# Kernel optimization log

Hardware: AMD Instinct MI355X
Metric: run time of the kernel (lower is better)

## Reference

```python
import jax, jax.numpy as jnp
import numpy as np

N = 50000
HID = 128
NH = 4
E_RES, E_SEQ, E_KNN = 100000, 100000, 200000
BN_EPS = 1e-5
NEG_SLOPE = 0.2


def _gat(h, src, dst, W, al, ar, resW, b):
    """DGL-style GATConv (eval mode: feat_drop off, residual=True, bias).
    h: (N, in), W/resW: (in, H*out), al/ar: (H, out), b: (H*out,)"""
    Hh, out = al.shape
    feat = (h @ W).reshape(N, Hh, out)                 # (N, H, out)
    el = jnp.sum(feat * al, axis=-1)                   # (N, H)
    er = jnp.sum(feat * ar, axis=-1)                   # (N, H)
    e = jax.nn.leaky_relu(el[src] + er[dst], NEG_SLOPE)  # (E, H)
    # edge softmax over incoming edges of each dst node (numerically stable)
    m = jax.ops.segment_max(e, dst, num_segments=N)    # (N, H)
    ex = jnp.exp(e - m[dst])
    s = jax.ops.segment_sum(ex, dst, num_segments=N)
    a = ex / s[dst]                                    # (E, H)
    msg = a[:, :, None] * feat[src]                    # (E, H, out)
    rst = jax.ops.segment_sum(msg, dst, num_segments=N)  # (N, H, out)
    return rst + (h @ resW).reshape(N, Hh, out) + b.reshape(1, Hh, out)


def _hetero(h, src_res, dst_res, src_seq, dst_seq, src_knn, dst_knn, W, al, ar, resW, b):
    # HeteroGraphConv with aggregate='sum' over relations, then mean over heads
    r = _gat(h, src_res, dst_res, W[0], al[0], ar[0], resW[0], b[0])
    r = r + _gat(h, src_seq, dst_seq, W[1], al[1], ar[1], resW[1], b[1])
    r = r + _gat(h, src_knn, dst_knn, W[2], al[2], ar[2], resW[2], b[2])
    return jnp.mean(r, axis=1)                         # (N, out)


def setup_inputs() -> dict:
    key = jax.random.key(0)
    ks = iter(jax.random.split(key, 32))
    inp = {}
    inp["x"] = jax.random.normal(next(ks), (N, HID), jnp.float32)
    inp["src_res"] = jax.random.randint(next(ks), (E_RES,), 0, N, jnp.int32)
    inp["dst_res"] = jax.random.randint(next(ks), (E_RES,), 0, N, jnp.int32)
    inp["src_seq"] = jax.random.randint(next(ks), (E_SEQ,), 0, N, jnp.int32)
    inp["dst_seq"] = jax.random.randint(next(ks), (E_SEQ,), 0, N, jnp.int32)
    inp["src_knn"] = jax.random.randint(next(ks), (E_KNN,), 0, N, jnp.int32)
    inp["dst_knn"] = jax.random.randint(next(ks), (E_KNN,), 0, N, jnp.int32)
    sc = 0.05
    for l in (0, 1):
        inp[f"W{l}"] = jax.random.normal(next(ks), (3, HID, NH * HID), jnp.float32) * sc
        inp[f"al{l}"] = jax.random.normal(next(ks), (3, NH, HID), jnp.float32) * sc
        inp[f"ar{l}"] = jax.random.normal(next(ks), (3, NH, HID), jnp.float32) * sc
        inp[f"resW{l}"] = jax.random.normal(next(ks), (3, HID, NH * HID), jnp.float32) * sc
        inp[f"b{l}"] = jax.random.normal(next(ks), (3, NH * HID), jnp.float32) * sc
    inp["fc_W"] = jax.random.normal(next(ks), (HID, HID), jnp.float32) * sc
    inp["fc_b"] = jax.random.normal(next(ks), (HID,), jnp.float32) * sc
    inp["bn_gamma"] = jnp.ones((HID,), jnp.float32)
    inp["bn_beta"] = jnp.zeros((HID,), jnp.float32)
    inp["bn_mean"] = jax.random.normal(next(ks), (HID,), jnp.float32) * sc
    inp["bn_var"] = jax.random.uniform(next(ks), (HID,), jnp.float32)
    return inp


def reference(x, src_res, dst_res, src_seq, dst_seq, src_knn, dst_knn,
              W0, al0, ar0, resW0, b0, W1, al1, ar1, resW1, b1,
              fc_W, fc_b, bn_gamma, bn_beta, bn_mean, bn_var):
    # layer 0: hetero GAT, head-mean, fc + ReLU + BatchNorm (eval), dropout=identity
    h = _hetero(x, src_res, dst_res, src_seq, dst_seq, src_knn, dst_knn,
                W0, al0, ar0, resW0, b0)
    h = jax.nn.relu(h @ fc_W + fc_b)
    h = (h - bn_mean) / jnp.sqrt(bn_var + BN_EPS) * bn_gamma + bn_beta
    # layer 1 (final): hetero GAT, head-mean
    out = _hetero(h, src_res, dst_res, src_seq, dst_seq, src_knn, dst_knn,
                  W1, al1, ar1, resW1, b1)
    return out
```

## Files before the change

kernel.cpp:

```cpp
#include <hip/hip_runtime.h>
#include <hip/hip_bf16.h>
#include <math.h>
#include <stdint.h>

#define NNODES 50000
#define SCHUNK 4096
#define AW 1664
#define XOFF 1536

typedef __bf16 bf16x8 __attribute__((ext_vector_type(8)));
typedef float f32x4 __attribute__((ext_vector_type(4)));
typedef unsigned short u16;
typedef unsigned int u32;

__device__ __forceinline__ float lrelu(float x){ return x >= 0.f ? x : 0.2f*x; }
__device__ __forceinline__ float lo2f(u32 v){ union{ u32 i; float f; } c; c.i = v<<16; return c.f; }
__device__ __forceinline__ float hi2f(u32 v){ union{ u32 i; float f; } c; c.i = v & 0xffff0000u; return c.f; }
__device__ __forceinline__ u16 f2b(float f){ __hip_bfloat16 h = __float2bfloat16(f); return *(u16*)&h; }
__device__ __forceinline__ u32 packbf(float a, float b){ return (u32)f2b(a) | ((u32)f2b(b) << 16); }

#define GLDS16(g, l) __builtin_amdgcn_global_load_lds( \
    (const __attribute__((address_space(1))) void*)(g), \
    (__attribute__((address_space(3))) void*)(l), 16, 0, 0)

__global__ void prep_all(const float* __restrict__ W0, const float* __restrict__ W1,
                         const float* __restrict__ resW0, const float* __restrict__ resW1,
                         const float* __restrict__ b0, const float* __restrict__ b1,
                         const float* __restrict__ al0, const float* __restrict__ ar0,
                         const float* __restrict__ al1, const float* __restrict__ ar1,
                         const float* __restrict__ fcW,
                         u16* __restrict__ Btb, float* __restrict__ biasf,
                         u16* __restrict__ wlb, u16* __restrict__ fcWtb,
                         int* __restrict__ cnt)
{
    int gid = blockIdx.x*blockDim.x + threadIdx.x;
    if (gid < 3*NNODES) cnt[gid] = 0;
    if (gid < 2*128*AW){
        int l = gid / (128*AW);
        int rem = gid - l*(128*AW);
        int c = rem / AW;
        int j = rem - c*AW;
        const float* W  = l ? W1 : W0;
        const float* rw = l ? resW1 : resW0;
        float v;
        if (j < XOFF){
            int r = j >> 9, h = (j >> 7) & 3, k = j & 127;
            v = 0.25f * W[(size_t)r*65536 + (size_t)k*512 + h*128 + c];
        } else {
            int k = j - XOFF;
            float s = 0.f;
            for (int r = 0; r < 3; ++r)
                for (int h = 0; h < 4; ++h)
                    s += rw[(size_t)r*65536 + (size_t)k*512 + h*128 + c];
            v = 0.25f * s;
        }
        Btb[gid] = f2b(v);
    }
    if (gid < 256){
        int l = gid >> 7, c = gid & 127;
        const float* bb = l ? b1 : b0;
        float s = 0.f;
        for (int r = 0; r < 3; ++r)
            for (int h = 0; h < 4; ++h)
                s += bb[r*512 + h*128 + c];
        biasf[gid] = 0.25f*s;
    }
    if (gid < 2*128*128){
        int l = gid >> 14;
        int col = (gid >> 7) & 127;
        int k = gid & 127;
        float v = 0.f;
        if (col < 24){
            int r = col >> 3, lr = (col >> 2) & 1, h = col & 3;
            const float* W = l ? W1 : W0;
            const float* av = l ? (lr ? ar1 : al1) : (lr ? ar0 : al0);
            const float* wrow = W + (size_t)r*65536 + (size_t)k*512 + h*128;
            const float* arow = av + r*512 + h*128;
            for (int cc = 0; cc < 128; ++cc) v += wrow[cc]*arow[cc];
        }
        wlb[gid] = f2b(v);
    }
    if (gid < 128*128){
        int k = gid & 127, n = gid >> 7;
        fcWtb[gid] = f2b(fcW[k*128 + n]);
    }
}

__global__ __launch_bounds__(256) void xprep_kernel(const float* __restrict__ x,
    u16* __restrict__ Ax, const u16* __restrict__ wl, float* __restrict__ el, int M)
{
    __shared__ u16 Xs[64*136];
    __shared__ u16 Ws[32*136];
    const int tid = threadIdx.x;
    const int row0 = blockIdx.x*64;
    #pragma unroll
    for (int p = 0; p < 2; ++p){
        int idx = tid + p*256;
        int c = idx >> 4, kc = (idx & 15)*8;
        float4 v = make_float4(0.f,0.f,0.f,0.f);
        if (c < 24) v = *(const float4*)(wl + c*128 + kc);
        *(float4*)&Ws[c*136 + kc] = v;
    }
    int r = tid >> 2, cq = (tid & 3)*32;
    int grow = row0 + r;
    if (grow < M){
        #pragma unroll
        for (int i = 0; i < 8; ++i){
            float4 v = *(const float4*)(x + (size_t)grow*128 + cq + i*4);
            ushort4 o;
            o.x = f2b(v.x); o.y = f2b(v.y); o.z = f2b(v.z); o.w = f2b(v.w);
            *(ushort4*)(Ax + (size_t)grow*AW + cq + i*4) = o;
            *(ushort4*)&Xs[r*136 + cq + i*4] = o;
        }
    } else {
        ushort4 z; z.x=0; z.y=0; z.z=0; z.w=0;
        #pragma unroll
        for (int i = 0; i < 8; ++i) *(ushort4*)&Xs[r*136 + cq + i*4] = z;
    }
    __syncthreads();
    const int lane = tid & 63, wave = tid >> 6;
    const int r16 = lane & 15, quad = lane >> 4;
    f32x4 acc0 = {}, acc1 = {};
    #pragma unroll
    for (int ks = 0; ks < 4; ++ks){
        int ko = ks*32 + quad*8;
        bf16x8 a  = *(const bf16x8*)&Xs[(wave*16 + r16)*136 + ko];
        bf16x8 b0 = *(const bf16x8*)&Ws[r16*136 + ko];
        bf16x8 b1 = *(const bf16x8*)&Ws[(16 + r16)*136 + ko];
        acc0 = __builtin_amdgcn_mfma_f32_16x16x32_bf16(a, b0, acc0, 0,0,0);
        acc1 = __builtin_amdgcn_mfma_f32_16x16x32_bf16(a, b1, acc1, 0,0,0);
    }
    #pragma unroll
    for (int p = 0; p < 4; ++p){
        int row = row0 + wave*16 + quad*4 + p;
        if (row < M){
            el[(size_t)row*32 + r16] = acc0[p];
            if (r16 < 8) el[(size_t)row*32 + 16 + r16] = acc1[p];
        }
    }
}

__global__ void hist_all(const int* __restrict__ d0, const int* __restrict__ d1,
                         const int* __restrict__ d2, int e0, int e1, int e2,
                         int* __restrict__ cnt)
{
    int g = blockIdx.x*blockDim.x + threadIdx.x;
    if (g >= e0 + e1 + e2) return;
    int rel, idx;
    if (g < e0){ rel = 0; idx = g; }
    else if (g < e0 + e1){ rel = 1; idx = g - e0; }
    else { rel = 2; idx = g - e0 - e1; }
    const int* d = rel == 0 ? d0 : (rel == 1 ? d1 : d2);
    atomicAdd(cnt + (size_t)rel*NNODES + d[idx], 1);
}

__global__ __launch_bounds__(256) void scan_part(const int* __restrict__ cnt_all,
                                                 int* __restrict__ partials, int Nn, int nblk)
{
    int rel = blockIdx.y, blk = blockIdx.x;
    const int* cnt = cnt_all + (size_t)rel*Nn;
    int tid = threadIdx.x;
    int i0 = blk*SCHUNK + tid*16;
    int s = 0;
    #pragma unroll
    for (int k = 0; k < 4; ++k){
        int idx = i0 + k*4;
        if (idx + 3 < Nn){ int4 v = *(const int4*)(cnt + idx); s += v.x+v.y+v.z+v.w; }
        else { for (int j = 0; j < 4; ++j) if (idx+j < Nn) s += cnt[idx+j]; }
    }
    #pragma unroll
    for (int off = 1; off < 64; off <<= 1) s += __shfl_xor(s, off);
    __shared__ int ws[4];
    if ((tid & 63) == 0) ws[tid>>6] = s;
    __syncthreads();
    if (tid == 0) partials[rel*nblk + blk] = ws[0]+ws[1]+ws[2]+ws[3];
}

__global__ __launch_bounds__(256) void scan_write(const int* __restrict__ cnt_all,
                                                  const int* __restrict__ partials,
                                                  int* __restrict__ rp_all, int* __restrict__ cur_all,
                                                  int Nn, int nblk)
{
    int rel = blockIdx.y, blk = blockIdx.x;
    const int* cnt = cnt_all + (size_t)rel*Nn;
    int* rp  = rp_all  + (size_t)rel*(Nn+1);
    int* cur = cur_all + (size_t)rel*Nn;
    int tid = threadIdx.x;
    __shared__ int sOff;
    __shared__ int wsum[4];
    if (tid == 0){
        int o = 0;
        for (int b = 0; b < blk; ++b) o += partials[rel*nblk + b];
        sOff = o;
        if (blk == 0){
            int t = 0;
            for (int b = 0; b < nblk; ++b) t += partials[rel*nblk + b];
            rp[Nn] = t;
        }
    }
    int i0 = blk*SCHUNK + tid*16;
    int v[16];
    int s = 0;
    #pragma unroll
    for (int k = 0; k < 16; ++k){
        int idx = i0 + k;
        v[k] = (idx < Nn) ? cnt[idx] : 0;
        s += v[k];
    }
    int lane = tid & 63;
    int incl = s;
    #pragma unroll
    for (int off = 1; off < 64; off <<= 1){
        int t = __shfl_up(incl, off);
        if (lane >= off) incl += t;
    }
    if (lane == 63) wsum[tid>>6] = incl;
    __syncthreads();
    int woff = 0;
    for (int w = 0; w < (tid>>6); ++w) woff += wsum[w];
    int ex = sOff + woff + incl - s;
    #pragma unroll
    for (int k = 0; k < 16; ++k){
        int idx = i0 + k;
        if (idx < Nn){ rp[idx] = ex; cur[idx] = ex; }
        ex += v[k];
    }
}

__global__ void scatter_all(const int* __restrict__ s0, const int* __restrict__ s1,
                            const int* __restrict__ s2,
                            const int* __restrict__ d0, const int* __restrict__ d1,
                            const int* __restrict__ d2, int e0, int e1, int e2,
                            int* __restrict__ cur, int* __restrict__ colb)
{
    int g = blockIdx.x*blockDim.x + threadIdx.x;
    if (g >= e0 + e1 + e2) return;
    int rel, idx, coff;
    if (g < e0){ rel = 0; idx = g; coff = 0; }
    else if (g < e0 + e1){ rel = 1; idx = g - e0; coff = e0; }
    else { rel = 2; idx = g - e0 - e1; coff = e0 + e1; }
    const int* sp = rel == 0 ? s0 : (rel == 1 ? s1 : s2);
    const int* dp = rel == 0 ? d0 : (rel == 1 ? d1 : d2);
    int d = dp[idx];
    int pos = atomicAdd(cur + (size_t)rel*NNODES + d, 1);
    colb[coff + pos] = sp[idx];
}

__global__ __launch_bounds__(256) void agg3(const int* __restrict__ rowp_all,
    const int* __restrict__ colb_all, int e0, int e01,
    const float* __restrict__ el_all,
    const u16* __restrict__ Ax, u16* __restrict__ Abuf, int Nn)
{
    const int rel = blockIdx.y;
    const int tid = threadIdx.x;
    const int o = tid & 15;
    const int n = (blockIdx.x*256 + tid) >> 4;
    if (n >= Nn) return;
    const int* rowp = rowp_all + (size_t)rel*(Nn+1);
    const int coff = (rel == 0) ? 0 : ((rel == 1) ? e0 : e01);
    const int* colb = colb_all + coff;
    u16* op = Abuf + (size_t)n*AW + rel*512 + o*8;

    int beg = rowp[n], end = rowp[n+1];
    if (beg >= end){
        uint4 z; z.x = 0; z.y = 0; z.z = 0; z.w = 0;
        #pragma unroll
        for (int h = 0; h < 4; ++h) *(uint4*)(op + h*128) = z;
        return;
    }
    float4 ed = *(const float4*)(el_all + (size_t)n*32 + rel*8 + 4);
    float acc[4][8] = {};
    float us0 = 0.f, us1 = 0.f, us2 = 0.f, us3 = 0.f;

    int sa = colb[beg];
    uint4 xa = *(const uint4*)(Ax + (size_t)sa*AW + o*8);
    float4 ea = *(const float4*)(el_all + (size_t)sa*32 + rel*8);
    int sb = sa; uint4 xb = xa; float4 eb = ea;
    if (beg + 1 < end){
        sb = colb[beg+1];
        xb = *(const uint4*)(Ax + (size_t)sb*AW + o*8);
        eb = *(const float4*)(el_all + (size_t)sb*32 + rel*8);
    }
    for (int j = beg; j < end; ++j){
        int sc = sb; uint4 xc = xb; float4 ec = eb;
        if (j + 2 < end){
            sc = colb[j+2];
            xc = *(const uint4*)(Ax + (size_t)sc*AW + o*8);
            ec = *(const float4*)(el_all + (size_t)sc*32 + rel*8);
        }
        float w0 = __expf(lrelu(ea.x + ed.x));
        float w1 = __expf(lrelu(ea.y + ed.y));
        float w2 = __expf(lrelu(ea.z + ed.z));
        float w3 = __expf(lrelu(ea.w + ed.w));
        us0 += w0; us1 += w1; us2 += w2; us3 += w3;
        float xv[8];
        xv[0] = lo2f(xa.x); xv[1] = hi2f(xa.x);
        xv[2] = lo2f(xa.y); xv[3] = hi2f(xa.y);
        xv[4] = lo2f(xa.z); xv[5] = hi2f(xa.z);
        xv[6] = lo2f(xa.w); xv[7] = hi2f(xa.w);
        #pragma unroll
        for (int c = 0; c < 8; ++c){
            acc[0][c] = fmaf(w0, xv[c], acc[0][c]);
            acc[1][c] = fmaf(w1, xv[c], acc[1][c]);
            acc[2][c] = fmaf(w2, xv[c], acc[2][c]);
            acc[3][c] = fmaf(w3, xv[c], acc[3][c]);
        }
        xa = xb; ea = eb; sb = sc; xb = xc; eb = ec;
    }
    float inv[4] = {1.f/us0, 1.f/us1, 1.f/us2, 1.f/us3};
    #pragma unroll
    for (int h = 0; h < 4; ++h){
        uint4 ov;
        ov.x = packbf(acc[h][0]*inv[h], acc[h][1]*inv[h]);
        ov.y = packbf(acc[h][2]*inv[h], acc[h][3]*inv[h]);
        ov.z = packbf(acc[h][4]*inv[h], acc[h][5]*inv[h]);
        ov.w = packbf(acc[h][6]*inv[h], acc[h][7]*inv[h]);
        *(uint4*)(op + h*128) = ov;
    }
}

template<int EPI, int FCF>
__global__ __launch_bounds__(256, 3) void gemm_f(
    const u16* __restrict__ A, int Astride, int K,
    const u16* __restrict__ Bt,
    float* __restrict__ Cf, u16* __restrict__ Cb, int Cstride, int M,
    const float* __restrict__ bias, const float* __restrict__ gamma,
    const float* __restrict__ beta, const float* __restrict__ mean,
    const float* __restrict__ var,
    const u16* __restrict__ wl, float* __restrict__ el,
    const u16* __restrict__ fcw, const float* __restrict__ fcb2)
{
    __shared__ u16 smem[FCF ? 26112 : 16384];
    const int tid = threadIdx.x;
    const int row0 = blockIdx.x*128;
    const int lane = tid & 63, wave = tid >> 6;
    const int wm = (wave >> 1)*64, wn = (wave & 1)*64;
    const int r16 = lane & 15, quad = lane >> 4;
    const int swzbase = r16 & 7;
    f32x4 acc[4][4] = {};

    const int r8 = lane >> 3, jc = lane & 7;
    const int soff = ((jc ^ r8) << 3);
    const u16* srcA[4];
    const u16* srcB[4];
    #pragma unroll
    for (int g = 0; g < 4; ++g){
        int gr = row0 + wave*32 + g*8 + r8;
        if (gr >= M) gr = M - 1;
        srcA[g] = A + (size_t)gr*Astride + soff;
        srcB[g] = Bt + (size_t)(wave*32 + g*8 + r8)*K + soff;
    }
    u16* As = smem;
    u16* Bs = smem + 8192;
    const int nk = K >> 6;

    for (int t = 0; t < nk; ++t){
        const int k0 = t << 6;
        #pragma unroll
        for (int g = 0; g < 4; ++g){
            GLDS16(srcA[g] + k0, As + wave*2048 + g*512);
            GLDS16(srcB[g] + k0, Bs + wave*2048 + g*512);
        }
        __syncthreads();
        #pragma unroll
        for (int ks = 0; ks < 2; ++ks){
            int swz = ((ks*4 + quad) ^ swzbase) << 3;
            bf16x8 a[4], b[4];
            #pragma unroll
            for (int i = 0; i < 4; ++i) a[i] = *(const bf16x8*)&As[(wm + i*16 + r16)*64 + swz];
            #pragma unroll
            for (int j = 0; j < 4; ++j) b[j] = *(const bf16x8*)&Bs[(wn + j*16 + r16)*64 + swz];
            #pragma unroll
            for (int i = 0; i < 4; ++i)
                #pragma unroll
                for (int j = 0; j < 4; ++j)
                    acc[i][j] = __builtin_amdgcn_mfma_f32_16x16x32_bf16(a[i], b[j], acc[i][j], 0,0,0);
        }
        __syncthreads();
    }

    if (!FCF){
        #pragma unroll
        for (int i = 0; i < 4; ++i){
            #pragma unroll
            for (int p = 0; p < 4; ++p){
                int row = row0 + wm + i*16 + quad*4 + p;
                #pragma unroll
                for (int j = 0; j < 4; ++j){
                    int col = wn + j*16 + r16;
                    float v = acc[i][j][p] + bias[col];
                    if (row < M){
                        if (EPI == 1) Cf[(size_t)row*Cstride + col] = v;
                        else          Cb[(size_t)row*Cstride + col] = f2b(v);
                    }
                }
            }
        }
    } else {
        u16* Cs = smem;
        u16* Ws = smem + 17408;
        #pragma unroll
        for (int i = 0; i < 4; ++i){
            #pragma unroll
            for (int p = 0; p < 4; ++p){
                int rl = wm + i*16 + quad*4 + p;
                #pragma unroll
                for (int j = 0; j < 4; ++j){
                    int col = wn + j*16 + r16;
                    Cs[rl*136 + col] = f2b(acc[i][j][p] + bias[col]);
                }
            }
        }
        __syncthreads();
        f32x4 fa[2][8] = {};
        #pragma unroll
        for (int hh = 0; hh < 2; ++hh){
            {
                int rr = tid >> 2, sg = (tid & 3)*32;
                const u16* src = fcw + (size_t)(hh*64 + rr)*128 + sg;
                #pragma unroll
                for (int q = 0; q < 4; ++q)
                    *(float4*)&Ws[rr*136 + sg + q*8] = *(const float4*)(src + q*8);
            }
            __syncthreads();
            #pragma unroll
            for (int ks = 0; ks < 4; ++ks){
                int ko = ks*32 + quad*8;
                #pragma unroll
                for (int i = 0; i < 2; ++i){
                    bf16x8 a = *(const bf16x8*)&Cs[(wave*32 + i*16 + r16)*136 + ko];
                    #pragma unroll
                    for (int jj = 0; jj < 4; ++jj){
                        bf16x8 b = *(const bf16x8*)&Ws[(jj*16 + r16)*136 + ko];
                        fa[i][hh*4+jj] = __builtin_amdgcn_mfma_f32_16x16x32_bf16(a, b, fa[i][hh*4+jj], 0,0,0);
                    }
                }
            }
            __syncthreads();
        }
        #pragma unroll
        for (int f = 0; f < 8; ++f){
            int col = f*16 + r16;
            float fb = fcb2[col];
            float mn = mean[col];
            float sc = gamma[col]*rsqrtf(var[col] + 1e-5f);
            float bt = beta[col];
            #pragma unroll
            for (int i = 0; i < 2; ++i){
                #pragma unroll
                for (int p = 0; p < 4; ++p){
                    int rl = wave*32 + i*16 + quad*4 + p;
                    int row = row0 + rl;
                    float v = fa[i][f][p] + fb;
                    v = fmaxf(v, 0.f);
                    v = (v - mn)*sc + bt;
                    u16 vb = f2b(v);
                    if (row < M) Cb[(size_t)row*Cstride + col] = vb;
                    Cs[rl*136 + col] = vb;
                }
            }
        }
        #pragma unroll
        for (int p = 0; p < 2; ++p){
            int idx = tid + p*256;
            int c = idx >> 4, kc = (idx & 15)*8;
            float4 v = make_float4(0.f,0.f,0.f,0.f);
            if (c < 24) v = *(const float4*)(wl + c*128 + kc);
            *(float4*)&Ws[c*136 + kc] = v;
        }
        __syncthreads();
        f32x4 e0[2] = {}, e1[2] = {};
        #pragma unroll
        for (int ks = 0; ks < 4; ++ks){
            int ko = ks*32 + quad*8;
            #pragma unroll
            for (int i = 0; i < 2; ++i){
                bf16x8 a  = *(const bf16x8*)&Cs[(wave*32 + i*16 + r16)*136 + ko];
                bf16x8 b0 = *(const bf16x8*)&Ws[r16*136 + ko];
                bf16x8 b1 = *(const bf16x8*)&Ws[(16 + r16)*136 + ko];
                e0[i] = __builtin_amdgcn_mfma_f32_16x16x32_bf16(a, b0, e0[i], 0,0,0);
                e1[i] = __builtin_amdgcn_mfma_f32_16x16x32_bf16(a, b1, e1[i], 0,0,0);
            }
        }
        #pragma unroll
        for (int i = 0; i < 2; ++i){
            #pragma unroll
            for (int p = 0; p < 4; ++p){
                int row = row0 + wave*32 + i*16 + quad*4 + p;
                if (row < M){
                    el[(size_t)row*32 + r16] = e0[i][p];
                    if (r16 < 8) el[(size_t)row*32 + 16 + r16] = e1[i][p];
                }
            }
        }
    }
}

static inline char* align256(char* p){ return (char*)(((uintptr_t)p + 255) & ~(uintptr_t)255); }

extern "C" void kernel_launch(void* const* d_in, const int* in_sizes, int n_in,
                              void* d_out, int out_size, void* d_ws, size_t ws_size,
                              hipStream_t stream)
{
    const float* x      = (const float*)d_in[0];
    const int* srcs[3]  = {(const int*)d_in[1], (const int*)d_in[3], (const int*)d_in[5]};
    const int* dsts[3]  = {(const int*)d_in[2], (const int*)d_in[4], (const int*)d_in[6]};
    const int  E[3]     = {in_sizes[1], in_sizes[3], in_sizes[5]};
    const float* W0     = (const float*)d_in[7];
    const float* al0    = (const float*)d_in[8];
    const float* ar0    = (const float*)d_in[9];
    const float* resW0  = (const float*)d_in[10];
    const float* b0     = (const float*)d_in[11];
    const float* W1     = (const float*)d_in[12];
    const float* al1    = (const float*)d_in[13];
    const float* ar1    = (const float*)d_in[14];
    const float* resW1  = (const float*)d_in[15];
    const float* b1     = (const float*)d_in[16];
    const float* fcW    = (const float*)d_in[17];
    const float* fcb    = (const float*)d_in[18];
    const float* gamma  = (const float*)d_in[19];
    const float* beta   = (const float*)d_in[20];
    const float* bmean  = (const float*)d_in[21];
    const float* bvar   = (const float*)d_in[22];
    float* out = (float*)d_out;

    char* p = (char*)d_ws;
    u16*   Abuf  = (u16*)p;   p += (size_t)NNODES*AW*2;    p = align256(p);
    float* el    = (float*)p; p += (size_t)NNODES*32*4;    p = align256(p);
    int*   cnt   = (int*)p;   p += (size_t)3*NNODES*4;     p = align256(p);
    int*   rowp  = (int*)p;   p += (size_t)3*(NNODES+1)*4; p = align256(p);
    int*   cur   = (int*)p;   p += (size_t)3*NNODES*4;     p = align256(p);
    int*   colb  = (int*)p;   p += (size_t)(E[0]+E[1]+E[2])*4; p = align256(p);
    u16*   Btb   = (u16*)p;   p += (size_t)2*128*AW*2;     p = align256(p);
    u16*   wlb   = (u16*)p;   p += (size_t)2*128*128*2;    p = align256(p);
    u16*   fcWtb = (u16*)p;   p += (size_t)128*128*2;      p = align256(p);
    float* biasf = (float*)p; p += (size_t)2*128*4;        p = align256(p);
    int*   parts = (int*)p;   p += (size_t)3*64*4;

    const int NBLK = (NNODES + SCHUNK - 1)/SCHUNK;
    const int MB64 = (NNODES + 63)/64;
    const int MBG  = (NNODES + 127)/128;
    const int AGGBLKS = (NNODES*16 + 255)/256;
    const int ETOT = E[0] + E[1] + E[2];
    dim3 blk(256);
    u16* Ax = Abuf + XOFF;

    prep_all<<<(2*128*AW + 255)/256, blk, 0, stream>>>(W0, W1, resW0, resW1, b0, b1,
                                                       al0, ar0, al1, ar1, fcW,
                                                       Btb, biasf, wlb, fcWtb, cnt);
    xprep_kernel<<<MB64, blk, 0, stream>>>(x, Ax, wlb, el, NNODES);
    hist_all<<<(ETOT + 255)/256, blk, 0, stream>>>(dsts[0], dsts[1], dsts[2], E[0], E[1], E[2], cnt);
    scan_part <<<dim3(NBLK,3), blk, 0, stream>>>(cnt, parts, NNODES, NBLK);
    scan_write<<<dim3(NBLK,3), blk, 0, stream>>>(cnt, parts, rowp, cur, NNODES, NBLK);
    scatter_all<<<(ETOT + 255)/256, blk, 0, stream>>>(srcs[0], srcs[1], srcs[2],
                                                      dsts[0], dsts[1], dsts[2],
                                                      E[0], E[1], E[2], cur, colb);

    agg3<<<dim3(AGGBLKS,3), blk, 0, stream>>>(rowp, colb, E[0], E[0]+E[1], el, Ax, Abuf, NNODES);
    gemm_f<0,1><<<MBG, blk, 0, stream>>>(Abuf, AW, AW, Btb, nullptr, Ax, AW, NNODES,
                                         biasf, gamma, beta, bmean, bvar,
                                         wlb + 16384, el, fcWtb, fcb);

    agg3<<<dim3(AGGBLKS,3), blk, 0, stream>>>(rowp, colb, E[0], E[0]+E[1], el, Ax, Abuf, NNODES);
    gemm_f<1,0><<<MBG, blk, 0, stream>>>(Abuf, AW, AW, Btb + (size_t)128*AW, out, nullptr, 128, NNODES,
                                         biasf + 128, nullptr, nullptr, nullptr, nullptr,
                                         nullptr, nullptr, nullptr, nullptr);
}
```

Baseline: 360.0 us.

## Merge scan kernels and cooperatively compute edge weights in aggregation

```diff
diff --git a/kernel.cpp b/kernel.cpp
--- a/kernel.cpp
+++ b/kernel.cpp
@@ -154,50 +154,29 @@
     atomicAdd(cnt + (size_t)rel*NNODES + d[idx], 1);
 }
 
-__global__ __launch_bounds__(256) void scan_part(const int* __restrict__ cnt_all,
-                                                 int* __restrict__ partials, int Nn, int nblk)
-{
-    int rel = blockIdx.y, blk = blockIdx.x;
-    const int* cnt = cnt_all + (size_t)rel*Nn;
-    int tid = threadIdx.x;
-    int i0 = blk*SCHUNK + tid*16;
-    int s = 0;
-    #pragma unroll
-    for (int k = 0; k < 4; ++k){
-        int idx = i0 + k*4;
-        if (idx + 3 < Nn){ int4 v = *(const int4*)(cnt + idx); s += v.x+v.y+v.z+v.w; }
-        else { for (int j = 0; j < 4; ++j) if (idx+j < Nn) s += cnt[idx+j]; }
-    }
-    #pragma unroll
-    for (int off = 1; off < 64; off <<= 1) s += __shfl_xor(s, off);
-    __shared__ int ws[4];
-    if ((tid & 63) == 0) ws[tid>>6] = s;
-    __syncthreads();
-    if (tid == 0) partials[rel*nblk + blk] = ws[0]+ws[1]+ws[2]+ws[3];
-}
-
-__global__ __launch_bounds__(256) void scan_write(const int* __restrict__ cnt_all,
-                                                  const int* __restrict__ partials,
-                                                  int* __restrict__ rp_all, int* __restrict__ cur_all,
-                                                  int Nn, int nblk)
+__global__ __launch_bounds__(256) void scan_all(const int* __restrict__ cnt_all,
+                                                int* __restrict__ rp_all, int* __restrict__ cur_all,
+                                                int Nn, int nblk)
 {
     int rel = blockIdx.y, blk = blockIdx.x;
     const int* cnt = cnt_all + (size_t)rel*Nn;
     int* rp  = rp_all  + (size_t)rel*(Nn+1);
     int* cur = cur_all + (size_t)rel*Nn;
     int tid = threadIdx.x;
-    __shared__ int sOff;
+    __shared__ int wsA[4];
     __shared__ int wsum[4];
-    if (tid == 0){
-        int o = 0;
-        for (int b = 0; b < blk; ++b) o += partials[rel*nblk + b];
-        sOff = o;
-        if (blk == 0){
-            int t = 0;
-            for (int b = 0; b < nblk; ++b) t += partials[rel*nblk + b];
-            rp[Nn] = t;
-        }
-    }
+    __shared__ int sOffS;
+    int pre = blk*SCHUNK;
+    int s0 = 0;
+    for (int i = tid*4; i < pre; i += 1024){
+        int4 v = *(const int4*)(cnt + i);
+        s0 += v.x + v.y + v.z + v.w;
+    }
+    #pragma unroll
+    for (int off = 1; off < 64; off <<= 1) s0 += __shfl_xor(s0, off);
+    if ((tid & 63) == 0) wsA[tid >> 6] = s0;
+    __syncthreads();
+    if (tid == 0) sOffS = wsA[0] + wsA[1] + wsA[2] + wsA[3];
     int i0 = blk*SCHUNK + tid*16;
     int v[16];
     int s = 0;
@@ -214,10 +193,11 @@
         int t = __shfl_up(incl, off);
         if (lane >= off) incl += t;
     }
-    if (lane == 63) wsum[tid>>6] = incl;
+    if (lane == 63) wsum[tid >> 6] = incl;
     __syncthreads();
+    int sOff = sOffS;
     int woff = 0;
-    for (int w = 0; w < (tid>>6); ++w) woff += wsum[w];
+    for (int w = 0; w < (tid >> 6); ++w) woff += wsum[w];
     int ex = sOff + woff + incl - s;
     #pragma unroll
     for (int k = 0; k < 16; ++k){
@@ -225,6 +205,8 @@
         if (idx < Nn){ rp[idx] = ex; cur[idx] = ex; }
         ex += v[k];
     }
+    if (blk == nblk - 1 && tid == 0)
+        rp[Nn] = sOff + wsum[0] + wsum[1] + wsum[2] + wsum[3];
 }
 
 __global__ void scatter_all(const int* __restrict__ s0, const int* __restrict__ s1,
@@ -253,7 +235,9 @@
 {
     const int rel = blockIdx.y;
     const int tid = threadIdx.x;
+    const int lane = tid & 63;
     const int o = tid & 15;
+    const int base = lane & 48;
     const int n = (blockIdx.x*256 + tid) >> 4;
     if (n >= Nn) return;
     const int* rowp = rowp_all + (size_t)rel*(Nn+1);
@@ -272,40 +256,57 @@
     float acc[4][8] = {};
     float us0 = 0.f, us1 = 0.f, us2 = 0.f, us3 = 0.f;
 
-    int sa = colb[beg];
-    uint4 xa = *(const uint4*)(Ax + (size_t)sa*AW + o*8);
-    float4 ea = *(const float4*)(el_all + (size_t)sa*32 + rel*8);
-    int sb = sa; uint4 xb = xa; float4 eb = ea;
-    if (beg + 1 < end){
-        sb = colb[beg+1];
-        xb = *(const uint4*)(Ax + (size_t)sb*AW + o*8);
-        eb = *(const float4*)(el_all + (size_t)sb*32 + rel*8);
-    }
-    for (int j = beg; j < end; ++j){
-        int sc = sb; uint4 xc = xb; float4 ec = eb;
-        if (j + 2 < end){
-            sc = colb[j+2];
-            xc = *(const uint4*)(Ax + (size_t)sc*AW + o*8);
-            ec = *(const float4*)(el_all + (size_t)sc*32 + rel*8);
-        }
-        float w0 = __expf(lrelu(ea.x + ed.x));
-        float w1 = __expf(lrelu(ea.y + ed.y));
-        float w2 = __expf(lrelu(ea.z + ed.z));
-        float w3 = __expf(lrelu(ea.w + ed.w));
-        us0 += w0; us1 += w1; us2 += w2; us3 += w3;
-        float xv[8];
-        xv[0] = lo2f(xa.x); xv[1] = hi2f(xa.x);
-        xv[2] = lo2f(xa.y); xv[3] = hi2f(xa.y);
-        xv[4] = lo2f(xa.z); xv[5] = hi2f(xa.z);
-        xv[6] = lo2f(xa.w); xv[7] = hi2f(xa.w);
-        #pragma unroll
-        for (int c = 0; c < 8; ++c){
-            acc[0][c] = fmaf(w0, xv[c], acc[0][c]);
-            acc[1][c] = fmaf(w1, xv[c], acc[1][c]);
-            acc[2][c] = fmaf(w2, xv[c], acc[2][c]);
-            acc[3][c] = fmaf(w3, xv[c], acc[3][c]);
-        }
-        xa = xb; ea = eb; sb = sc; xb = xc; eb = ec;
+    for (int eb = beg; eb < end; eb += 16){
+        int rem = end - eb;
+        int cnt16 = rem < 16 ? rem : 16;
+        bool val = (o < cnt16);
+        int s_l = 0;
+        if (val) s_l = colb[eb + o];
+        float wl0 = 0.f, wl1 = 0.f, wl2 = 0.f, wl3 = 0.f;
+        if (val){
+            float4 e_l = *(const float4*)(el_all + (size_t)s_l*32 + rel*8);
+            wl0 = __expf(lrelu(e_l.x + ed.x));
+            wl1 = __expf(lrelu(e_l.y + ed.y));
+            wl2 = __expf(lrelu(e_l.z + ed.z));
+            wl3 = __expf(lrelu(e_l.w + ed.w));
+        }
+        us0 += wl0; us1 += wl1; us2 += wl2; us3 += wl3;
+        int st0 = __shfl(s_l, base);
+        uint4 xa = *(const uint4*)(Ax + (size_t)st0*AW + o*8);
+        uint4 xb = xa;
+        if (cnt16 > 1){
+            int st1 = __shfl(s_l, base + 1);
+            xb = *(const uint4*)(Ax + (size_t)st1*AW + o*8);
+        }
+        for (int t = 0; t < cnt16; ++t){
+            uint4 xc = xb;
+            if (t + 2 < cnt16){
+                int st2 = __shfl(s_l, base + t + 2);
+                xc = *(const uint4*)(Ax + (size_t)st2*AW + o*8);
+            }
+            float w0 = __shfl(wl0, base + t);
+            float w1 = __shfl(wl1, base + t);
+            float w2 = __shfl(wl2, base + t);
+            float w3 = __shfl(wl3, base + t);
+            float xv[8];
+            xv[0] = lo2f(xa.x); xv[1] = hi2f(xa.x);
+            xv[2] = lo2f(xa.y); xv[3] = hi2f(xa.y);
+            xv[4] = lo2f(xa.z); xv[5] = hi2f(xa.z);
+            xv[6] = lo2f(xa.w); xv[7] = hi2f(xa.w);
+            #pragma unroll
+            for (int c = 0; c < 8; ++c){
+                acc[0][c] = fmaf(w0, xv[c], acc[0][c]);
+                acc[1][c] = fmaf(w1, xv[c], acc[1][c]);
+                acc[2][c] = fmaf(w2, xv[c], acc[2][c]);
+                acc[3][c] = fmaf(w3, xv[c], acc[3][c]);
+            }
+            xa = xb; xb = xc;
+        }
+    }
+    #pragma unroll
+    for (int off = 1; off < 16; off <<= 1){
+        us0 += __shfl_xor(us0, off); us1 += __shfl_xor(us1, off);
+        us2 += __shfl_xor(us2, off); us3 += __shfl_xor(us3, off);
     }
     float inv[4] = {1.f/us0, 1.f/us1, 1.f/us2, 1.f/us3};
     #pragma unroll
@@ -535,7 +536,6 @@
     u16*   wlb   = (u16*)p;   p += (size_t)2*128*128*2;    p = align256(p);
     u16*   fcWtb = (u16*)p;   p += (size_t)128*128*2;      p = align256(p);
     float* biasf = (float*)p; p += (size_t)2*128*4;        p = align256(p);
-    int*   parts = (int*)p;   p += (size_t)3*64*4;
 
     const int NBLK = (NNODES + SCHUNK - 1)/SCHUNK;
     const int MB64 = (NNODES + 63)/64;
@@ -550,8 +550,7 @@
                                                        Btb, biasf, wlb, fcWtb, cnt);
     xprep_kernel<<<MB64, blk, 0, stream>>>(x, Ax, wlb, el, NNODES);
     hist_all<<<(ETOT + 255)/256, blk, 0, stream>>>(dsts[0], dsts[1], dsts[2], E[0], E[1], E[2], cnt);
-    scan_part <<<dim3(NBLK,3), blk, 0, stream>>>(cnt, parts, NNODES, NBLK);
-    scan_write<<<dim3(NBLK,3), blk, 0, stream>>>(cnt, parts, rowp, cur, NNODES, NBLK);
+    scan_all<<<dim3(NBLK,3), blk, 0, stream>>>(cnt, rowp, cur, NNODES, NBLK);
     scatter_all<<<(ETOT + 255)/256, blk, 0, stream>>>(srcs[0], srcs[1], srcs[2],
                                                       dsts[0], dsts[1], dsts[2],
                                                       E[0], E[1], E[2], cur, colb);
```

Result: no change. 361.0 us (+0.3%).
